# Optimization experiments

Hardware: AMD Instinct MI355X
Metric: run time of the kernel (lower is better)

## Reference

```python
import jax, jax.numpy as jnp
import numpy as np

DEPTH = 18                      # perfect binary tree depth -> N = 2**DEPTH - 1 nodes
N_NODES = 2 ** DEPTH - 1        # 262143
VOCAB, E, H = 2048, 64, 64


def setup_inputs() -> dict:
    key = jax.random.key(0)
    ks = jax.random.split(key, 10)
    token_ids = jax.random.randint(ks[0], (N_NODES,), 0, VOCAB, dtype=jnp.int32)
    emb = jax.random.normal(ks[1], (VOCAB, E), dtype=jnp.float32)
    emb = emb.at[0].set(0.0)  # padding_idx=0 row is zero in torch
    s = 0.1  # keep gates out of hard saturation
    return {
        "token_ids": token_ids,
        "emb": emb,
        "W_iou": jax.random.normal(ks[2], (3 * H, E), dtype=jnp.float32) * s,
        "b_Wiou": jnp.zeros((3 * H,), dtype=jnp.float32),
        "U_iou": jax.random.normal(ks[3], (3 * H, 2 * H), dtype=jnp.float32) * s,
        "b_Uiou": jnp.zeros((3 * H,), dtype=jnp.float32),
        "W_f": jax.random.normal(ks[4], (2 * H, E), dtype=jnp.float32) * s,
        "b_Wf": jnp.zeros((2 * H,), dtype=jnp.float32),
        "U_f": jax.random.normal(ks[5], (2 * H, 2 * H), dtype=jnp.float32) * s,
        "b_Uf": jnp.zeros((2 * H,), dtype=jnp.float32),
        "depth": DEPTH,
    }


def _tree_lstm(token_ids, emb, W_iou, b_Wiou, U_iou, b_Uiou, W_f, b_Wf, U_f, b_Uf, depth):
    """Level-synchronous bottom-up Binary TreeLSTM over a perfect binary tree.

    Node i has children 2i+1 (left), 2i+2 (right); level l occupies
    indices [2**l - 1, 2**(l+1) - 2]. Children of level-l node k sit at
    offsets 2k, 2k+1 of level l+1, so a reshape gives (left, right) pairs.
    """
    Hd = W_f.shape[0] // 2
    h = c = None
    for l in range(depth - 1, -1, -1):
        start, n = 2 ** l - 1, 2 ** l
        x = emb[token_ids[start:start + n]]                    # [n, E]
        if h is None:  # leaves: zero left/right states (both children zero)
            h_cat = jnp.zeros((n, 2 * Hd), dtype=x.dtype)
            c_lr = jnp.zeros((n, 2, Hd), dtype=x.dtype)
        else:
            h_cat = h.reshape(n, 2 * Hd)                        # [h_l | h_r]
            c_lr = c.reshape(n, 2, Hd)
        iou = jax.nn.sigmoid(x @ W_iou.T + b_Wiou + h_cat @ U_iou.T + b_Uiou)
        i_g, o_g, u_g = jnp.split(iou, 3, axis=1)
        u_g = jnp.tanh(u_g)  # faithful: tanh(sigmoid(u_pre)) as in the source
        f = jax.nn.sigmoid(x @ W_f.T + b_Wf + h_cat @ U_f.T + b_Uf)
        f_l, f_r = f[:, :Hd], f[:, Hd:]
        c = i_g * u_g + f_l * c_lr[:, 0] + f_r * c_lr[:, 1]
        h = o_g * jnp.tanh(c)
    return jnp.stack([h, c])  # [2, 1, H]: root (h, c)


def reference(token_ids, emb, W_iou, b_Wiou, U_iou, b_Uiou, W_f, b_Wf, U_f, b_Uf, depth):
    return _tree_lstm(token_ids, emb, W_iou, b_Wiou, U_iou, b_Uiou,
                      W_f, b_Wf, U_f, b_Uf, depth)
```

## Files before the change

kernel.cpp:

```cpp
#include <hip/hip_runtime.h>

typedef __bf16 bf16;
typedef __bf16 bf16x8 __attribute__((ext_vector_type(8)));
typedef float f32x4 __attribute__((ext_vector_type(4)));

#define DEPTH   18
#define N_NODES ((1 << DEPTH) - 1)
#define KDIM    192
#define RDIM    320
#define A_PAD   200
#define LOG2E   1.4426950408889634f

__device__ __forceinline__ float rcpf(float x) { return __builtin_amdgcn_rcpf(x); }
__device__ __forceinline__ float sig2(float p)  { return rcpf(1.f + exp2f(-p)); }
__device__ __forceinline__ float tanhf_(float x){ return 2.f * rcpf(1.f + exp2f(-2.f * LOG2E * x)) - 1.f; }

__device__ __forceinline__ void gates(const f32x4* acc,
        const float4& bI, const float4& bO, const float4& bU,
        const float4& bL, const float4& bR,
        const float4& cl, const float4& cr, float4& c4, float4& h4) {
    const float* pbI = &bI.x; const float* pbO = &bO.x; const float* pbU = &bU.x;
    const float* pbL = &bL.x; const float* pbR = &bR.x;
    const float* pcl = &cl.x; const float* pcr = &cr.x;
    float* pc4 = &c4.x; float* ph4 = &h4.x;
#pragma unroll
    for (int r = 0; r < 4; r++) {
        float i_g = sig2(acc[0][r] + pbI[r]);
        float o_g = sig2(acc[1][r] + pbO[r]);
        float u_g = tanhf_(sig2(acc[2][r] + pbU[r]));
        float fl  = sig2(acc[3][r] + pbL[r]);
        float fr  = sig2(acc[4][r] + pbR[r]);
        float c = i_g * u_g + fl * pcl[r] + fr * pcr[r];
        pc4[r] = c;
        ph4[r] = o_g * tanhf_(c);
    }
}

__global__ void prep_all(const float* __restrict__ emb,
                     const float* __restrict__ W_iou, const float* __restrict__ U_iou,
                     const float* __restrict__ W_f,   const float* __restrict__ U_f,
                     const float* __restrict__ b_Wiou, const float* __restrict__ b_Uiou,
                     const float* __restrict__ b_Wf,   const float* __restrict__ b_Uf,
                     bf16* __restrict__ Wcat, float* __restrict__ bias, bf16* __restrict__ emb16,
                     bf16* __restrict__ leafH, float* __restrict__ leafC) {
    __shared__ __align__(16) bf16 Wl[192 * 72];
    __shared__ __align__(16) bf16 Al[64 * 72];
    const int blk = blockIdx.x, tid = threadIdx.x;
    if (blk < 512) {
        int t = blk * 256 + tid;
        emb16[t] = (bf16)emb[t];
        if (t < RDIM * KDIM) {
            int r = t / KDIM, k = t % KDIM;
            float v;
            if (r < 192) v = (k < 64) ? W_iou[r * 64 + k] : U_iou[r * 128 + (k - 64)];
            else { int rr = r - 192; v = (k < 64) ? W_f[rr * 64 + k] : U_f[rr * 128 + (k - 64)]; }
            Wcat[t] = (bf16)(v * LOG2E);
        }
        if (t < RDIM)
            bias[t] = ((t < 192) ? (b_Wiou[t] + b_Uiou[t]) : (b_Wf[t - 192] + b_Uf[t - 192])) * LOG2E;
        return;
    }
    const int v0 = (blk - 512) * 64;
    for (int i = tid; i < 192 * 64; i += 256) {
        int r = i >> 6, k = i & 63;
        Wl[r * 72 + k] = (bf16)(W_iou[i] * LOG2E);
    }
    for (int i = tid; i < 64 * 64; i += 256) {
        int r = i >> 6, k = i & 63;
        Al[r * 72 + k] = (bf16)emb[(v0 << 6) + i];
    }
    __syncthreads();
    const int wave = tid >> 6, lane = tid & 63;
    const int l15 = lane & 15, quad = lane >> 4;
    const int jw = (wave & 3) * 16, jb = jw + quad * 4;

    f32x4 acc[4][3];
#pragma unroll
    for (int t = 0; t < 4; t++)
#pragma unroll
        for (int g = 0; g < 3; g++) acc[t][g] = (f32x4){0.f, 0.f, 0.f, 0.f};
#pragma unroll
    for (int kb = 0; kb < 2; kb++) {
        bf16x8 wfrag[3], nfrag[4];
#pragma unroll
        for (int g = 0; g < 3; g++)
            wfrag[g] = *(const bf16x8*)(&Wl[(g * 64 + jw + l15) * 72 + kb * 32 + quad * 8]);
#pragma unroll
        for (int t = 0; t < 4; t++)
            nfrag[t] = *(const bf16x8*)(&Al[(t * 16 + l15) * 72 + kb * 32 + quad * 8]);
#pragma unroll
        for (int t = 0; t < 4; t++)
#pragma unroll
            for (int g = 0; g < 3; g++)
                acc[t][g] = __builtin_amdgcn_mfma_f32_16x16x32_bf16(wfrag[g], nfrag[t], acc[t][g], 0, 0, 0);
    }
    float4 bW, bU_;
    bW = *(const float4*)(b_Wiou + jb);       bU_ = *(const float4*)(b_Uiou + jb);
    float4 bI = make_float4((bW.x + bU_.x) * LOG2E, (bW.y + bU_.y) * LOG2E, (bW.z + bU_.z) * LOG2E, (bW.w + bU_.w) * LOG2E);
    bW = *(const float4*)(b_Wiou + 64 + jb);  bU_ = *(const float4*)(b_Uiou + 64 + jb);
    float4 bO = make_float4((bW.x + bU_.x) * LOG2E, (bW.y + bU_.y) * LOG2E, (bW.z + bU_.z) * LOG2E, (bW.w + bU_.w) * LOG2E);
    bW = *(const float4*)(b_Wiou + 128 + jb); bU_ = *(const float4*)(b_Uiou + 128 + jb);
    float4 bU = make_float4((bW.x + bU_.x) * LOG2E, (bW.y + bU_.y) * LOG2E, (bW.z + bU_.z) * LOG2E, (bW.w + bU_.w) * LOG2E);
    const float* pbI = &bI.x; const float* pbO = &bO.x; const float* pbU = &bU.x;
#pragma unroll
    for (int t = 0; t < 4; t++) {
        int v = v0 + t * 16 + l15;
        float4 c4; float* pc4 = &c4.x;
        union { bf16 h[4]; uint2 u; } hp;
#pragma unroll
        for (int r = 0; r < 4; r++) {
            float i_g = sig2(acc[t][0][r] + pbI[r]);
            float o_g = sig2(acc[t][1][r] + pbO[r]);
            float u_g = tanhf_(sig2(acc[t][2][r] + pbU[r]));
            float c = i_g * u_g;
            pc4[r] = c;
            hp.h[r] = (bf16)(o_g * tanhf_(c));
        }
        *(float4*)(leafC + (size_t)v * 64 + jb) = c4;
        *(uint2*)(leafH + (size_t)v * 64 + jb) = hp.u;
    }
}

__global__ __launch_bounds__(512, 2) void big_pass(
        const bf16* __restrict__ Wcat, const float* __restrict__ bias,
        const bf16* __restrict__ emb16, const int* __restrict__ token_ids,
        const bf16* __restrict__ leafH, const float* __restrict__ leafC,
        bf16* __restrict__ H, float* __restrict__ c_buf) {
    __shared__ __align__(16) bf16 A0[256 * A_PAD];
    __shared__ __align__(16) bf16 A1[128 * A_PAD];
    const int tid = threadIdx.x, blk = blockIdx.x;
    const int wave = tid >> 6, lane = tid & 63;
    const int l15 = lane & 15, quad = lane >> 4;
    const int wj = wave & 3, wt = wave >> 2;
    const int jw = wj * 16, jb = jw + quad * 4;

    const int base16 = 65535 + blk * 256;

    for (int ch = tid; ch < 256 * 8; ch += 512) {
        int row = ch >> 3, k8 = (ch & 7) << 3;
        int tok = token_ids[base16 + row];
        *(uint4*)&A0[row * A_PAD + k8] = *(const uint4*)(emb16 + tok * 64 + k8);
    }
    for (int ch = tid; ch < 256 * 16; ch += 512) {
        int row = ch >> 4, half = (ch >> 3) & 1, k8 = (ch & 7) << 3;
        int tok = token_ids[2 * (base16 + row) + 1 + half];
        *(uint4*)&A0[row * A_PAD + 64 + half * 64 + k8] = *(const uint4*)(leafH + (size_t)tok * 64 + k8);
    }

    int tkl16[8], tkr16[8];
#pragma unroll
    for (int q = 0; q < 8; q++) {
        int idx = (wt + 2 * q) * 16 + l15;
        int gn = base16 + idx;
        tkl16[q] = token_ids[2 * gn + 1];
        tkr16[q] = token_ids[2 * gn + 2];
    }

    bf16x8 Wf[5][6];
#pragma unroll
    for (int g = 0; g < 5; g++)
#pragma unroll
        for (int kb = 0; kb < 6; kb++)
            Wf[g][kb] = *(const bf16x8*)(Wcat + (g * 64 + jw + l15) * KDIM + kb * 32 + quad * 8);

    const float4 bI = *(const float4*)(bias + jb);
    const float4 bO = *(const float4*)(bias + 64 + jb);
    const float4 bU = *(const float4*)(bias + 128 + jb);
    const float4 bL = *(const float4*)(bias + 192 + jb);
    const float4 bR = *(const float4*)(bias + 256 + jb);
    __syncthreads();

#pragma unroll
    for (int q = 0; q < 8; q++) {
        const int idx = (wt + 2 * q) * 16 + l15;
        const int gn = base16 + idx;
        float4 cl = *(const float4*)(leafC + (size_t)tkl16[q] * 64 + jb);
        float4 cr = *(const float4*)(leafC + (size_t)tkr16[q] * 64 + jb);
        f32x4 acc[5];
#pragma unroll
        for (int g = 0; g < 5; g++) acc[g] = (f32x4){0.f, 0.f, 0.f, 0.f};
#pragma unroll
        for (int kb = 0; kb < 6; kb++) {
            bf16x8 nf = *(const bf16x8*)(&A0[idx * A_PAD + kb * 32 + quad * 8]);
#pragma unroll
            for (int g = 0; g < 5; g++)
                acc[g] = __builtin_amdgcn_mfma_f32_16x16x32_bf16(Wf[g][kb], nf, acc[g], 0, 0, 0);
        }
        float4 c4, h4;
        gates(acc, bI, bO, bU, bL, bR, cl, cr, c4, h4);
        union { bf16 h[4]; uint2 u; } hp;
        const float* ph4 = &h4.x;
#pragma unroll
        for (int r = 0; r < 4; r++) hp.h[r] = (bf16)ph4[r];
        *(float4*)(c_buf + (size_t)gn * 64 + jb) = c4;
        *(uint2*)(&A1[(idx >> 1) * A_PAD + 64 + (idx & 1) * 64 + jb]) = hp.u;
    }
    for (int ch = tid; ch < 128 * 8; ch += 512) {
        int row = ch >> 3, k8 = (ch & 7) << 3;
        int tok = token_ids[32767 + blk * 128 + row];
        *(uint4*)&A1[row * A_PAD + k8] = *(const uint4*)(emb16 + tok * 64 + k8);
    }
    __syncthreads();

    bf16* Acur = A1;
    bf16* Anx  = A0;
    for (int l = 15; l >= 8; l--) {
        const int m = 1 << (l - 8);
        const int s = (1 << l) - 1, o = blk * m;
        const int T = (m + 15) >> 4;
        for (int ti = wt; ti < T; ti += 2) {
            int idx0 = ti * 16 + l15;
            int idx = idx0 < m ? idx0 : m - 1;
            int gn = s + o + idx;
            float4 cl = *(const float4*)(c_buf + (size_t)(2 * gn + 1) * 64 + jb);
            float4 cr = *(const float4*)(c_buf + (size_t)(2 * gn + 2) * 64 + jb);
            f32x4 acc[5];
#pragma unroll
            for (int g = 0; g < 5; g++) acc[g] = (f32x4){0.f, 0.f, 0.f, 0.f};
#pragma unroll
            for (int kb = 0; kb < 6; kb++) {
                bf16x8 nf = *(const bf16x8*)(&Acur[idx * A_PAD + kb * 32 + quad * 8]);
#pragma unroll
                for (int g = 0; g < 5; g++)
                    acc[g] = __builtin_amdgcn_mfma_f32_16x16x32_bf16(Wf[g][kb], nf, acc[g], 0, 0, 0);
            }
            float4 c4, h4;
            gates(acc, bI, bO, bU, bL, bR, cl, cr, c4, h4);
            if (idx0 < m) {
                union { bf16 h[4]; uint2 u; } hp;
                const float* ph4 = &h4.x;
#pragma unroll
                for (int r = 0; r < 4; r++) hp.h[r] = (bf16)ph4[r];
                *(float4*)(c_buf + (size_t)gn * 64 + jb) = c4;
                if (l > 8)
                    *(uint2*)(&Anx[(idx >> 1) * A_PAD + 64 + (idx & 1) * 64 + jb]) = hp.u;
                else
                    *(uint2*)(H + (size_t)gn * 64 + jb) = hp.u;
            }
        }
        if (l > 8) {
            int mn = m >> 1, sn = (1 << (l - 1)) - 1, on = blk * mn;
            for (int ch = tid; ch < mn * 8; ch += 512) {
                int row = ch >> 3, k8 = (ch & 7) << 3;
                int tok = token_ids[sn + on + row];
                *(uint4*)&Anx[row * A_PAD + k8] = *(const uint4*)(emb16 + tok * 64 + k8);
            }
        }
        __syncthreads();
        bf16* tmp = Acur; Acur = Anx; Anx = tmp;
    }
}

__global__ __launch_bounds__(512) void tail_pass(
        const bf16* __restrict__ Wcat, const float* __restrict__ bias,
        const bf16* __restrict__ emb16, const int* __restrict__ token_ids,
        const bf16* __restrict__ H, const float* __restrict__ c_buf,
        float* __restrict__ out) {
    __shared__ __align__(16) bf16 A[255 * A_PAD];
    __shared__ __align__(16) float C0[128 * 68];
    __shared__ __align__(16) float C1[64 * 68];
    const int tid = threadIdx.x;
    const int wave = tid >> 6, lane = tid & 63;
    const int l15 = lane & 15, quad = lane >> 4;
    const int wj = wave & 3, wt = wave >> 2;
    const int jw = wj * 16, jb = jw + quad * 4;

    float4 cl7[4], cr7[4];
#pragma unroll
    for (int q = 0; q < 4; q++) {
        int idx = (wt + 2 * q) * 16 + l15;
        int gn = 127 + idx;
        cl7[q] = *(const float4*)(c_buf + (size_t)(2 * gn + 1) * 64 + jb);
        cr7[q] = *(const float4*)(c_buf + (size_t)(2 * gn + 2) * 64 + jb);
    }

    for (int ch = tid; ch < 255 * 8; ch += 512) {
        int row = ch >> 3, k8 = (ch & 7) << 3;
        int l = 31 - __clz(255 - row);
        int idx = row - 256 + (2 << l);
        int gn = (1 << l) - 1 + idx;
        int tok = token_ids[gn];
        *(uint4*)&A[row * A_PAD + k8] = *(const uint4*)(emb16 + tok * 64 + k8);
    }
    for (int ch = tid; ch < 128 * 16; ch += 512) {
        int row = ch >> 4, k8 = (ch & 15) << 3;
        *(uint4*)&A[row * A_PAD + 64 + k8] =
            *(const uint4*)(H + (size_t)(255 + 2 * row) * 64 + k8);
    }

    bf16x8 Wf[5][6];
#pragma unroll
    for (int g = 0; g < 5; g++)
#pragma unroll
        for (int kb = 0; kb < 6; kb++)
            Wf[g][kb] = *(const bf16x8*)(Wcat + (g * 64 + jw + l15) * KDIM + kb * 32 + quad * 8);

    const float4 bI = *(const float4*)(bias + jb);
    const float4 bO = *(const float4*)(bias + 64 + jb);
    const float4 bU = *(const float4*)(bias + 128 + jb);
    const float4 bL = *(const float4*)(bias + 192 + jb);
    const float4 bR = *(const float4*)(bias + 256 + jb);
    __syncthreads();

#pragma unroll
    for (int q = 0; q < 4; q++) {
        const int idx = (wt + 2 * q) * 16 + l15;
        f32x4 acc[5];
#pragma unroll
        for (int g = 0; g < 5; g++) acc[g] = (f32x4){0.f, 0.f, 0.f, 0.f};
#pragma unroll
        for (int kb = 0; kb < 6; kb++) {
            bf16x8 nf = *(const bf16x8*)(&A[idx * A_PAD + kb * 32 + quad * 8]);
#pragma unroll
            for (int g = 0; g < 5; g++)
                acc[g] = __builtin_amdgcn_mfma_f32_16x16x32_bf16(Wf[g][kb], nf, acc[g], 0, 0, 0);
        }
        float4 c4, h4;
        gates(acc, bI, bO, bU, bL, bR, cl7[q], cr7[q], c4, h4);
        union { bf16 h[4]; uint2 u; } hp;
        const float* ph4 = &h4.x;
#pragma unroll
        for (int r = 0; r < 4; r++) hp.h[r] = (bf16)ph4[r];
        *(float4*)(C0 + idx * 68 + jb) = c4;
        *(uint2*)(&A[(128 + (idx >> 1)) * A_PAD + 64 + (idx & 1) * 64 + jb]) = hp.u;
    }
    __syncthreads();

    float* Ccur = C0;
    float* Cnx  = C1;
    for (int l = 6; l >= 0; l--) {
        const int n = 1 << l;
        const int off  = 256 - 2 * n;
        const int offn = 256 - n;
        const int T = (n + 15) >> 4;
        for (int ti = wt; ti < T; ti += 2) {
            int idx0 = ti * 16 + l15;
            int idx = idx0 < n ? idx0 : n - 1;
            float4 cl = *(const float4*)(Ccur + (2 * idx) * 68 + jb);
            float4 cr = *(const float4*)(Ccur + (2 * idx + 1) * 68 + jb);
            f32x4 acc[5];
#pragma unroll
            for (int g = 0; g < 5; g++) acc[g] = (f32x4){0.f, 0.f, 0.f, 0.f};
#pragma unroll
            for (int kb = 0; kb < 6; kb++) {
                bf16x8 nf = *(const bf16x8*)(&A[(off + idx) * A_PAD + kb * 32 + quad * 8]);
#pragma unroll
                for (int g = 0; g < 5; g++)
                    acc[g] = __builtin_amdgcn_mfma_f32_16x16x32_bf16(Wf[g][kb], nf, acc[g], 0, 0, 0);
            }
            float4 c4, h4;
            gates(acc, bI, bO, bU, bL, bR, cl, cr, c4, h4);
            if (idx0 < n) {
                if (l > 0) {
                    union { bf16 h[4]; uint2 u; } hp;
                    const float* ph4 = &h4.x;
#pragma unroll
                    for (int r = 0; r < 4; r++) hp.h[r] = (bf16)ph4[r];
                    *(float4*)(Cnx + idx * 68 + jb) = c4;
                    *(uint2*)(&A[(offn + (idx >> 1)) * A_PAD + 64 + (idx & 1) * 64 + jb]) = hp.u;
                } else {
                    *(float4*)(out + jb) = h4;
                    *(float4*)(out + 64 + jb) = c4;
                }
            }
        }
        __syncthreads();
        float* t = Ccur; Ccur = Cnx; Cnx = t;
    }
}

extern "C" void kernel_launch(void* const* d_in, const int* in_sizes, int n_in,
                              void* d_out, int out_size, void* d_ws, size_t ws_size,
                              hipStream_t stream) {
    const int*   token_ids = (const int*)d_in[0];
    const float* emb       = (const float*)d_in[1];
    const float* W_iou     = (const float*)d_in[2];
    const float* b_Wiou    = (const float*)d_in[3];
    const float* U_iou     = (const float*)d_in[4];
    const float* b_Uiou    = (const float*)d_in[5];
    const float* W_f       = (const float*)d_in[6];
    const float* b_Wf      = (const float*)d_in[7];
    const float* U_f       = (const float*)d_in[8];
    const float* b_Uf      = (const float*)d_in[9];
    float* out = (float*)d_out;

    char* ws = (char*)d_ws;
    bf16*  Wcat  = (bf16*)ws;
    float* bias  = (float*)(ws + 122880);
    bf16*  emb16 = (bf16*)(ws + 124160);
    bf16*  leafH = (bf16*)(ws + 386304);
    float* leafC = (float*)(ws + 648448);
    bf16*  H     = (bf16*)(ws + 1172736);
    float* c_buf = (float*)(ws + 34727040);

    prep_all<<<544, 256, 0, stream>>>(emb, W_iou, U_iou, W_f, U_f,
                                      b_Wiou, b_Uiou, b_Wf, b_Uf,
                                      Wcat, bias, emb16, leafH, leafC);
    big_pass<<<256, 512, 0, stream>>>(Wcat, bias, emb16, token_ids, leafH, leafC, H, c_buf);
    tail_pass<<<1, 512, 0, stream>>>(Wcat, bias, emb16, token_ids, H, c_buf, out);
}
```

Baseline: 167.3 us.

## Split big_pass across 512 blocks and add separate level-8 kernel

Halves the subtree each big_pass block owns (128 nodes at level 16, stopping at level 9), doubling the grid to 512 blocks with higher launch-bound occupancy. A new small level8_pass kernel computes level 8 from the H/c buffers. Weight fragments are no longer held in registers; they are reloaded from global/cache inside each MFMA loop to cut register pressure. The aim is to fill more CUs on MI355X. The cost is extra weight-load traffic and one more kernel launch.

Result: slower. 376.0 us (+124.8%).

```diff
diff --git a/kernel.cpp b/kernel.cpp
--- a/kernel.cpp
+++ b/kernel.cpp
@@ -121,47 +121,41 @@
     }
 }
 
-__global__ __launch_bounds__(512, 2) void big_pass(
+__global__ __launch_bounds__(512, 4) void big_pass(
         const bf16* __restrict__ Wcat, const float* __restrict__ bias,
         const bf16* __restrict__ emb16, const int* __restrict__ token_ids,
         const bf16* __restrict__ leafH, const float* __restrict__ leafC,
         bf16* __restrict__ H, float* __restrict__ c_buf) {
-    __shared__ __align__(16) bf16 A0[256 * A_PAD];
-    __shared__ __align__(16) bf16 A1[128 * A_PAD];
+    __shared__ __align__(16) bf16 A0[128 * A_PAD];
+    __shared__ __align__(16) bf16 A1[64 * A_PAD];
     const int tid = threadIdx.x, blk = blockIdx.x;
     const int wave = tid >> 6, lane = tid & 63;
     const int l15 = lane & 15, quad = lane >> 4;
     const int wj = wave & 3, wt = wave >> 2;
     const int jw = wj * 16, jb = jw + quad * 4;
 
-    const int base16 = 65535 + blk * 256;
-
-    for (int ch = tid; ch < 256 * 8; ch += 512) {
+    const int base16 = 65535 + blk * 128;
+    const bf16* Wb = Wcat + (size_t)(jw + l15) * KDIM + quad * 8;
+
+    for (int ch = tid; ch < 128 * 8; ch += 512) {
         int row = ch >> 3, k8 = (ch & 7) << 3;
         int tok = token_ids[base16 + row];
         *(uint4*)&A0[row * A_PAD + k8] = *(const uint4*)(emb16 + tok * 64 + k8);
     }
-    for (int ch = tid; ch < 256 * 16; ch += 512) {
+    for (int ch = tid; ch < 128 * 16; ch += 512) {
         int row = ch >> 4, half = (ch >> 3) & 1, k8 = (ch & 7) << 3;
         int tok = token_ids[2 * (base16 + row) + 1 + half];
         *(uint4*)&A0[row * A_PAD + 64 + half * 64 + k8] = *(const uint4*)(leafH + (size_t)tok * 64 + k8);
     }
 
-    int tkl16[8], tkr16[8];
-#pragma unroll
-    for (int q = 0; q < 8; q++) {
+    int tkl16[4], tkr16[4];
+#pragma unroll
+    for (int q = 0; q < 4; q++) {
         int idx = (wt + 2 * q) * 16 + l15;
         int gn = base16 + idx;
         tkl16[q] = token_ids[2 * gn + 1];
         tkr16[q] = token_ids[2 * gn + 2];
     }
-
-    bf16x8 Wf[5][6];
-#pragma unroll
-    for (int g = 0; g < 5; g++)
-#pragma unroll
-        for (int kb = 0; kb < 6; kb++)
-            Wf[g][kb] = *(const bf16x8*)(Wcat + (g * 64 + jw + l15) * KDIM + kb * 32 + quad * 8);
 
     const float4 bI = *(const float4*)(bias + jb);
     const float4 bO = *(const float4*)(bias + 64 + jb);
@@ -171,7 +165,7 @@
     __syncthreads();
 
 #pragma unroll
-    for (int q = 0; q < 8; q++) {
+    for (int q = 0; q < 4; q++) {
         const int idx = (wt + 2 * q) * 16 + l15;
         const int gn = base16 + idx;
         float4 cl = *(const float4*)(leafC + (size_t)tkl16[q] * 64 + jb);
@@ -184,7 +178,8 @@
             bf16x8 nf = *(const bf16x8*)(&A0[idx * A_PAD + kb * 32 + quad * 8]);
 #pragma unroll
             for (int g = 0; g < 5; g++)
-                acc[g] = __builtin_amdgcn_mfma_f32_16x16x32_bf16(Wf[g][kb], nf, acc[g], 0, 0, 0);
+                acc[g] = __builtin_amdgcn_mfma_f32_16x16x32_bf16(
+                    *(const bf16x8*)(Wb + (size_t)g * 64 * KDIM + kb * 32), nf, acc[g], 0, 0, 0);
         }
         float4 c4, h4;
         gates(acc, bI, bO, bU, bL, bR, cl, cr, c4, h4);
@@ -195,17 +190,17 @@
         *(float4*)(c_buf + (size_t)gn * 64 + jb) = c4;
         *(uint2*)(&A1[(idx >> 1) * A_PAD + 64 + (idx & 1) * 64 + jb]) = hp.u;
     }
-    for (int ch = tid; ch < 128 * 8; ch += 512) {
+    for (int ch = tid; ch < 64 * 8; ch += 512) {
         int row = ch >> 3, k8 = (ch & 7) << 3;
-        int tok = token_ids[32767 + blk * 128 + row];
+        int tok = token_ids[32767 + blk * 64 + row];
         *(uint4*)&A1[row * A_PAD + k8] = *(const uint4*)(emb16 + tok * 64 + k8);
     }
     __syncthreads();
 
     bf16* Acur = A1;
     bf16* Anx  = A0;
-    for (int l = 15; l >= 8; l--) {
-        const int m = 1 << (l - 8);
+    for (int l = 15; l >= 9; l--) {
+        const int m = 1 << (l - 9);
         const int s = (1 << l) - 1, o = blk * m;
         const int T = (m + 15) >> 4;
         for (int ti = wt; ti < T; ti += 2) {
@@ -222,7 +217,8 @@
                 bf16x8 nf = *(const bf16x8*)(&Acur[idx * A_PAD + kb * 32 + quad * 8]);
 #pragma unroll
                 for (int g = 0; g < 5; g++)
-                    acc[g] = __builtin_amdgcn_mfma_f32_16x16x32_bf16(Wf[g][kb], nf, acc[g], 0, 0, 0);
+                    acc[g] = __builtin_amdgcn_mfma_f32_16x16x32_bf16(
+                        *(const bf16x8*)(Wb + (size_t)g * 64 * KDIM + kb * 32), nf, acc[g], 0, 0, 0);
             }
             float4 c4, h4;
             gates(acc, bI, bO, bU, bL, bR, cl, cr, c4, h4);
@@ -232,13 +228,13 @@
 #pragma unroll
                 for (int r = 0; r < 4; r++) hp.h[r] = (bf16)ph4[r];
                 *(float4*)(c_buf + (size_t)gn * 64 + jb) = c4;
-                if (l > 8)
+                if (l > 9)
                     *(uint2*)(&Anx[(idx >> 1) * A_PAD + 64 + (idx & 1) * 64 + jb]) = hp.u;
                 else
                     *(uint2*)(H + (size_t)gn * 64 + jb) = hp.u;
             }
         }
-        if (l > 8) {
+        if (l > 9) {
             int mn = m >> 1, sn = (1 << (l - 1)) - 1, on = blk * mn;
             for (int ch = tid; ch < mn * 8; ch += 512) {
                 int row = ch >> 3, k8 = (ch & 7) << 3;
@@ -249,6 +245,60 @@
         __syncthreads();
         bf16* tmp = Acur; Acur = Anx; Anx = tmp;
     }
+}
+
+__global__ __launch_bounds__(256) void level8_pass(
+        const bf16* __restrict__ Wcat, const float* __restrict__ bias,
+        const bf16* __restrict__ emb16, const int* __restrict__ token_ids,
+        bf16* __restrict__ H, float* __restrict__ c_buf) {
+    __shared__ __align__(16) bf16 A[16 * A_PAD];
+    const int tid = threadIdx.x, blk = blockIdx.x;
+    const int p0 = blk * 16;
+    const int wave = tid >> 6, lane = tid & 63;
+    const int l15 = lane & 15, quad = lane >> 4;
+    const int jw = wave * 16, jb = jw + quad * 4;
+
+    for (int ch = tid; ch < 16 * 8; ch += 256) {
+        int row = ch >> 3, k8 = (ch & 7) << 3;
+        int tok = token_ids[255 + p0 + row];
+        *(uint4*)&A[row * A_PAD + k8] = *(const uint4*)(emb16 + tok * 64 + k8);
+    }
+    for (int ch = tid; ch < 16 * 16; ch += 256) {
+        int row = ch >> 4, k8 = (ch & 15) << 3;
+        *(uint4*)&A[row * A_PAD + 64 + k8] =
+            *(const uint4*)(H + (size_t)(511 + 2 * (p0 + row)) * 64 + k8);
+    }
+    __syncthreads();
+
+    const bf16* Wb = Wcat + (size_t)(jw + l15) * KDIM + quad * 8;
+    const float4 bI = *(const float4*)(bias + jb);
+    const float4 bO = *(const float4*)(bias + 64 + jb);
+    const float4 bU = *(const float4*)(bias + 128 + jb);
+    const float4 bL = *(const float4*)(bias + 192 + jb);
+    const float4 bR = *(const float4*)(bias + 256 + jb);
+
+    const int idx = l15, p = p0 + idx, gn = 255 + p;
+    float4 cl = *(const float4*)(c_buf + (size_t)(511 + 2 * p) * 64 + jb);
+    float4 cr = *(const float4*)(c_buf + (size_t)(512 + 2 * p) * 64 + jb);
+    f32x4 acc[5];
+#pragma unroll
+    for (int g = 0; g < 5; g++) acc[g] = (f32x4){0.f, 0.f, 0.f, 0.f};
+#pragma unroll
+    for (int kb = 0; kb < 6; kb++) {
+        bf16x8 nf = *(const bf16x8*)(&A[idx * A_PAD + kb * 32 + quad * 8]);
+#pragma unroll
+        for (int g = 0; g < 5; g++)
+            acc[g] = __builtin_amdgcn_mfma_f32_16x16x32_bf16(
+                *(const bf16x8*)(Wb + (size_t)g * 64 * KDIM + kb * 32), nf, acc[g], 0, 0, 0);
+    }
+    float4 c4, h4;
+    gates(acc, bI, bO, bU, bL, bR, cl, cr, c4, h4);
+    union { bf16 h[4]; uint2 u; } hp;
+    const float* ph4 = &h4.x;
+#pragma unroll
+    for (int r = 0; r < 4; r++) hp.h[r] = (bf16)ph4[r];
+    *(float4*)(c_buf + (size_t)gn * 64 + jb) = c4;
+    *(uint2*)(H + (size_t)gn * 64 + jb) = hp.u;
 }
 
 __global__ __launch_bounds__(512) void tail_pass(
@@ -396,6 +446,7 @@
     prep_all<<<544, 256, 0, stream>>>(emb, W_iou, U_iou, W_f, U_f,
                                       b_Wiou, b_Uiou, b_Wf, b_Uf,
                                       Wcat, bias, emb16, leafH, leafC);
-    big_pass<<<256, 512, 0, stream>>>(Wcat, bias, emb16, token_ids, leafH, leafC, H, c_buf);
+    big_pass<<<512, 512, 0, stream>>>(Wcat, bias, emb16, token_ids, leafH, leafC, H, c_buf);
+    level8_pass<<<16, 256, 0, stream>>>(Wcat, bias, emb16, token_ids, H, c_buf);
     tail_pass<<<1, 512, 0, stream>>>(Wcat, bias, emb16, token_ids, H, c_buf, out);
 }
```

## Keep intermediate cell states in LDS across levels and prefetch child loads

Applied to the files above, without the earlier changes.

For levels 14 through 9 of big_pass, child cell states are now kept in shared memory, placed after the active activation rows. Only level 16, level 8 and the level-15 reads still go through the global c_buf, which removes most global round-trips between levels. Per-level work is moved into a templated level_phase that issues all child c loads and the next level's embedding-token index loads before the MFMA loop. The leaf-parent phase is split into two groups so its loads are batched and the level-15 embedding gather overlaps the compute. Launch bounds drop to one block per CU and the c_buf workspace offset is compacted, which adds register pressure and relies on careful LDS aliasing.

Result: faster. 162.1 us (median of 2 runs) (-3.1%).

```diff
diff --git a/kernel.cpp b/kernel.cpp
--- a/kernel.cpp
+++ b/kernel.cpp
@@ -121,7 +121,83 @@
     }
 }
 
-__global__ __launch_bounds__(512, 2) void big_pass(
+template<int NQ, bool CGLOB>
+__device__ __forceinline__ void level_phase(
+        int l, int blk, int tid, int wt, int l15, int quad, int jb,
+        const bf16x8 (&Wf)[5][6],
+        const float4& bI, const float4& bO, const float4& bU,
+        const float4& bL, const float4& bR,
+        bf16* Acur, bf16* Anx,
+        const bf16* __restrict__ emb16, const int* __restrict__ token_ids,
+        bf16* __restrict__ H, float* __restrict__ c_buf)
+{
+    const int m = 1 << (l - 8);
+    const int s = (1 << l) - 1, o = blk * m;
+    const int T = (m + 15) >> 4;
+    const int mn = m >> 1;
+    const float* Cin = (const float*)(Acur + m * A_PAD);
+
+    float4 pcl[NQ], pcr[NQ];
+    int pidx[NQ], pgn[NQ]; bool pact[NQ];
+#pragma unroll
+    for (int q = 0; q < NQ; q++) {
+        int ti = wt + 2 * q;
+        int idx0 = ti * 16 + l15;
+        bool act = (ti < T) && (idx0 < m);
+        int idx = act ? idx0 : 0;
+        pidx[q] = idx; pact[q] = act; pgn[q] = s + o + idx;
+        if (CGLOB) {
+            pcl[q] = *(const float4*)(c_buf + (size_t)(2 * pgn[q] + 1) * 64 + jb);
+            pcr[q] = *(const float4*)(c_buf + (size_t)(2 * pgn[q] + 2) * 64 + jb);
+        } else {
+            pcl[q] = *(const float4*)(Cin + (2 * idx) * 68 + jb);
+            pcr[q] = *(const float4*)(Cin + (2 * idx + 1) * 68 + jb);
+        }
+    }
+
+    int tok = 0;
+    const int srow = tid >> 3, sk8 = (tid & 7) << 3;
+    const bool sact = (l > 8) && (tid < mn * 8);
+    if (sact) tok = token_ids[(1 << (l - 1)) - 1 + blk * mn + srow];
+
+    float* Cout = (float*)(Anx + mn * A_PAD);
+#pragma unroll
+    for (int q = 0; q < NQ; q++) {
+        f32x4 acc[5];
+#pragma unroll
+        for (int g = 0; g < 5; g++) acc[g] = (f32x4){0.f, 0.f, 0.f, 0.f};
+#pragma unroll
+        for (int kb = 0; kb < 6; kb++) {
+            bf16x8 nf = *(const bf16x8*)(&Acur[pidx[q] * A_PAD + kb * 32 + quad * 8]);
+#pragma unroll
+            for (int g = 0; g < 5; g++)
+                acc[g] = __builtin_amdgcn_mfma_f32_16x16x32_bf16(Wf[g][kb], nf, acc[g], 0, 0, 0);
+        }
+        float4 c4, h4;
+        gates(acc, bI, bO, bU, bL, bR, pcl[q], pcr[q], c4, h4);
+        if (pact[q]) {
+            union { bf16 h[4]; uint2 u; } hp;
+            const float* ph4 = &h4.x;
+#pragma unroll
+            for (int r = 0; r < 4; r++) hp.h[r] = (bf16)ph4[r];
+            if (l > 8) {
+                *(float4*)(Cout + pidx[q] * 68 + jb) = c4;
+                *(uint2*)(&Anx[(pidx[q] >> 1) * A_PAD + 64 + (pidx[q] & 1) * 64 + jb]) = hp.u;
+            } else {
+                *(float4*)(c_buf + (size_t)pgn[q] * 64 + jb) = c4;
+                *(uint2*)(H + (size_t)pgn[q] * 64 + jb) = hp.u;
+            }
+        }
+    }
+
+    if (sact) {
+        uint4 g = *(const uint4*)(emb16 + (size_t)tok * 64 + sk8);
+        *(uint4*)(&Anx[srow * A_PAD + sk8]) = g;
+    }
+    __syncthreads();
+}
+
+__global__ __launch_bounds__(512, 1) void big_pass(
         const bf16* __restrict__ Wcat, const float* __restrict__ bias,
         const bf16* __restrict__ emb16, const int* __restrict__ token_ids,
         const bf16* __restrict__ leafH, const float* __restrict__ leafC,
@@ -155,6 +231,10 @@
         tkl16[q] = token_ids[2 * gn + 1];
         tkr16[q] = token_ids[2 * gn + 2];
     }
+    const int rowa = tid >> 3, k8a = (tid & 7) << 3;
+    const int rowb = (tid + 512) >> 3, k8b = k8a;
+    const int tok15a = token_ids[32767 + blk * 128 + rowa];
+    const int tok15b = token_ids[32767 + blk * 128 + rowb];
 
     bf16x8 Wf[5][6];
 #pragma unroll
@@ -171,83 +251,57 @@
     __syncthreads();
 
 #pragma unroll
-    for (int q = 0; q < 8; q++) {
-        const int idx = (wt + 2 * q) * 16 + l15;
-        const int gn = base16 + idx;
-        float4 cl = *(const float4*)(leafC + (size_t)tkl16[q] * 64 + jb);
-        float4 cr = *(const float4*)(leafC + (size_t)tkr16[q] * 64 + jb);
-        f32x4 acc[5];
-#pragma unroll
-        for (int g = 0; g < 5; g++) acc[g] = (f32x4){0.f, 0.f, 0.f, 0.f};
-#pragma unroll
-        for (int kb = 0; kb < 6; kb++) {
-            bf16x8 nf = *(const bf16x8*)(&A0[idx * A_PAD + kb * 32 + quad * 8]);
-#pragma unroll
-            for (int g = 0; g < 5; g++)
-                acc[g] = __builtin_amdgcn_mfma_f32_16x16x32_bf16(Wf[g][kb], nf, acc[g], 0, 0, 0);
-        }
-        float4 c4, h4;
-        gates(acc, bI, bO, bU, bL, bR, cl, cr, c4, h4);
-        union { bf16 h[4]; uint2 u; } hp;
-        const float* ph4 = &h4.x;
-#pragma unroll
-        for (int r = 0; r < 4; r++) hp.h[r] = (bf16)ph4[r];
-        *(float4*)(c_buf + (size_t)gn * 64 + jb) = c4;
-        *(uint2*)(&A1[(idx >> 1) * A_PAD + 64 + (idx & 1) * 64 + jb]) = hp.u;
-    }
-    for (int ch = tid; ch < 128 * 8; ch += 512) {
-        int row = ch >> 3, k8 = (ch & 7) << 3;
-        int tok = token_ids[32767 + blk * 128 + row];
-        *(uint4*)&A1[row * A_PAD + k8] = *(const uint4*)(emb16 + tok * 64 + k8);
-    }
-    __syncthreads();
-
-    bf16* Acur = A1;
-    bf16* Anx  = A0;
-    for (int l = 15; l >= 8; l--) {
-        const int m = 1 << (l - 8);
-        const int s = (1 << l) - 1, o = blk * m;
-        const int T = (m + 15) >> 4;
-        for (int ti = wt; ti < T; ti += 2) {
-            int idx0 = ti * 16 + l15;
-            int idx = idx0 < m ? idx0 : m - 1;
-            int gn = s + o + idx;
-            float4 cl = *(const float4*)(c_buf + (size_t)(2 * gn + 1) * 64 + jb);
-            float4 cr = *(const float4*)(c_buf + (size_t)(2 * gn + 2) * 64 + jb);
+    for (int grp = 0; grp < 2; grp++) {
+        float4 cl4[4], cr4[4];
+#pragma unroll
+        for (int q = 0; q < 4; q++) {
+            cl4[q] = *(const float4*)(leafC + (size_t)tkl16[grp * 4 + q] * 64 + jb);
+            cr4[q] = *(const float4*)(leafC + (size_t)tkr16[grp * 4 + q] * 64 + jb);
+        }
+#pragma unroll
+        for (int q = 0; q < 4; q++) {
+            const int idx = (wt + 2 * (grp * 4 + q)) * 16 + l15;
+            const int gn = base16 + idx;
             f32x4 acc[5];
 #pragma unroll
             for (int g = 0; g < 5; g++) acc[g] = (f32x4){0.f, 0.f, 0.f, 0.f};
 #pragma unroll
             for (int kb = 0; kb < 6; kb++) {
-                bf16x8 nf = *(const bf16x8*)(&Acur[idx * A_PAD + kb * 32 + quad * 8]);
+                bf16x8 nf = *(const bf16x8*)(&A0[idx * A_PAD + kb * 32 + quad * 8]);
 #pragma unroll
                 for (int g = 0; g < 5; g++)
                     acc[g] = __builtin_amdgcn_mfma_f32_16x16x32_bf16(Wf[g][kb], nf, acc[g], 0, 0, 0);
             }
             float4 c4, h4;
-            gates(acc, bI, bO, bU, bL, bR, cl, cr, c4, h4);
-            if (idx0 < m) {
-                union { bf16 h[4]; uint2 u; } hp;
-                const float* ph4 = &h4.x;
-#pragma unroll
-                for (int r = 0; r < 4; r++) hp.h[r] = (bf16)ph4[r];
-                *(float4*)(c_buf + (size_t)gn * 64 + jb) = c4;
-                if (l > 8)
-                    *(uint2*)(&Anx[(idx >> 1) * A_PAD + 64 + (idx & 1) * 64 + jb]) = hp.u;
-                else
-                    *(uint2*)(H + (size_t)gn * 64 + jb) = hp.u;
-            }
-        }
-        if (l > 8) {
-            int mn = m >> 1, sn = (1 << (l - 1)) - 1, on = blk * mn;
-            for (int ch = tid; ch < mn * 8; ch += 512) {
-                int row = ch >> 3, k8 = (ch & 7) << 3;
-                int tok = token_ids[sn + on + row];
-                *(uint4*)&Anx[row * A_PAD + k8] = *(const uint4*)(emb16 + tok * 64 + k8);
-            }
-        }
-        __syncthreads();
-        bf16* tmp = Acur; Acur = Anx; Anx = tmp;
+            gates(acc, bI, bO, bU, bL, bR, cl4[q], cr4[q], c4, h4);
+            union { bf16 h[4]; uint2 u; } hp;
+            const float* ph4 = &h4.x;
+#pragma unroll
+            for (int r = 0; r < 4; r++) hp.h[r] = (bf16)ph4[r];
+            *(float4*)(c_buf + (size_t)gn * 64 + jb) = c4;
+            *(uint2*)(&A1[(idx >> 1) * A_PAD + 64 + (idx & 1) * 64 + jb]) = hp.u;
+        }
+        if (grp == 0) {
+            uint4 ga = *(const uint4*)(emb16 + (size_t)tok15a * 64 + k8a);
+            uint4 gb = *(const uint4*)(emb16 + (size_t)tok15b * 64 + k8b);
+            *(uint4*)(&A1[rowa * A_PAD + k8a]) = ga;
+            *(uint4*)(&A1[rowb * A_PAD + k8b]) = gb;
+        }
+    }
+    __syncthreads();
+
+    bf16* Acur = A1;
+    bf16* Anx  = A0;
+    level_phase<4, true >(15, blk, tid, wt, l15, quad, jb, Wf, bI, bO, bU, bL, bR,
+                          Acur, Anx, emb16, token_ids, H, c_buf);
+    { bf16* t = Acur; Acur = Anx; Anx = t; }
+    level_phase<2, false>(14, blk, tid, wt, l15, quad, jb, Wf, bI, bO, bU, bL, bR,
+                          Acur, Anx, emb16, token_ids, H, c_buf);
+    { bf16* t = Acur; Acur = Anx; Anx = t; }
+    for (int l = 13; l >= 8; l--) {
+        level_phase<1, false>(l, blk, tid, wt, l15, quad, jb, Wf, bI, bO, bU, bL, bR,
+                              Acur, Anx, emb16, token_ids, H, c_buf);
+        bf16* t = Acur; Acur = Anx; Anx = t;
     }
 }
 
@@ -391,7 +445,7 @@
     bf16*  leafH = (bf16*)(ws + 386304);
     float* leafC = (float*)(ws + 648448);
     bf16*  H     = (bf16*)(ws + 1172736);
-    float* c_buf = (float*)(ws + 34727040);
+    float* c_buf = (float*)(ws + 1238272);
 
     prep_all<<<544, 256, 0, stream>>>(emb, W_iou, U_iou, W_f, U_f,
                                       b_Wiou, b_Uiou, b_Wf, b_Uf,
```
